# Performance work log

Hardware: AMD Instinct MI355X
Metric: run time of the kernel (lower is better)

The kernel has to match this reference:

```python
import jax, jax.numpy as jnp
import numpy as np

B, S, D, V, OOV = 32, 1024, 512, 50000, 1000
BN_EPS = 1e-5


def setup_inputs() -> dict:
    key = jax.random.key(0)
    ks = jax.random.split(key, 24)
    std = 0.02
    inp = {
        'dec_output': jax.random.normal(ks[0], (B, 1, D), jnp.float32),
        'dec_hid_h': jax.random.normal(ks[1], (1, B, D), jnp.float32),
        'dec_hid_c': jax.random.normal(ks[2], (1, B, D), jnp.float32),
        'dec_inp': jax.random.normal(ks[3], (B, 1, D), jnp.float32),
        'enc_op': jax.random.normal(ks[4], (B, S, 2 * D), jnp.float32),
        'enc_op1': jax.random.normal(ks[5], (B, S, 2 * D), jnp.float32),
        'src_inp': jax.random.randint(ks[6], (B, S), 0, V, jnp.int64) if jax.config.jax_enable_x64 else jax.random.randint(ks[6], (B, S), 0, V, jnp.int32),
        # mod_dec_op: Linear(2D -> 2D) with bias
        'W_dec': jax.random.normal(ks[7], (2 * D, 2 * D), jnp.float32) * std,
        'b_dec': jax.random.normal(ks[8], (2 * D,), jnp.float32) * std,
        # get_attn: Linear(2D -> 1), no bias
        'w_attn': jax.random.normal(ks[9], (2 * D,), jnp.float32) * std,
        # get_vocab: Linear(3D -> D) then Linear(D -> V-OOV)
        'W_v1': jax.random.normal(ks[10], (D, 3 * D), jnp.float32) * std,
        'b_v1': jax.random.normal(ks[11], (D,), jnp.float32) * std,
        'W_v2': jax.random.normal(ks[12], (V - OOV, D), jnp.float32) * std,
        'b_v2': jax.random.normal(ks[13], (V - OOV,), jnp.float32) * std,
        # p_gen: sigmoid(Linear([context(2D); dec_state(2D); dec_inp(D)] -> 1))
        'W_p': jax.random.normal(ks[14], (1, 5 * D), jnp.float32) * std,
        'b_p': jax.random.normal(ks[15], (1,), jnp.float32) * std,
        # BatchNorm1d(2D), eval mode
        'bn_gamma': jnp.ones((2 * D,), jnp.float32),
        'bn_beta': jnp.zeros((2 * D,), jnp.float32),
        'bn_mean': jax.random.normal(ks[16], (2 * D,), jnp.float32) * 0.1,
        'bn_var': jax.random.uniform(ks[17], (2 * D,), jnp.float32, 0.5, 1.5),
    }
    return inp


def reference(dec_output, dec_hid_h, dec_hid_c, dec_inp, enc_op, enc_op1, src_inp,
              W_dec, b_dec, w_attn, W_v1, b_v1, W_v2, b_v2, W_p, b_p,
              bn_gamma, bn_beta, bn_mean, bn_var):
    # dec_op: [B, 2D] = [h_b ; c_b]
    dec_op = jnp.concatenate([dec_hid_h[0], dec_hid_c[0]], axis=-1)
    dec_op1 = dec_op @ W_dec.T + b_dec                              # [B, 2D]
    features = jnp.tanh(enc_op1 + dec_op1[:, None, :])              # [B, S, 2D]
    attn = jax.nn.softmax(jnp.einsum('bsd,d->bs', features, w_attn), axis=-1)
    mask = (src_inp != 0).astype(attn.dtype)
    attn = attn * mask
    attn = attn / jnp.sum(attn, axis=1, keepdims=True)              # renormalize
    context = jnp.einsum('bs,bsd->bd', attn, enc_op)                # [B, 2D]
    context = (context - bn_mean) * jax.lax.rsqrt(bn_var + BN_EPS) * bn_gamma + bn_beta
    temp = jnp.concatenate([dec_output[:, 0, :], context], axis=-1)  # [B, 3D]
    logits = (temp @ W_v1.T + b_v1) @ W_v2.T + b_v2                 # [B, V-OOV]
    p_vocab = jax.nn.softmax(logits, axis=-1)
    p_vocab = jnp.concatenate([p_vocab, jnp.zeros((p_vocab.shape[0], OOV), p_vocab.dtype)], axis=-1)
    pg_in = jnp.concatenate([context, dec_op, dec_inp[:, 0, :]], axis=-1)  # [B, 5D]
    p_gen = jax.nn.sigmoid(pg_in @ W_p.T + b_p)                     # [B, 1]
    src_attn = (1.0 - p_gen) * attn                                  # [B, S]
    p_final = p_gen * p_vocab                                        # [B, V]
    rows = jnp.arange(p_final.shape[0])[:, None]
    p_final = p_final.at[rows, src_inp].add(src_attn)
    p_final = p_final + (p_final == 0).astype(p_final.dtype) * 1e-12
    return (p_final, attn, context)
```

## Files before the change

### kernel.cpp

```cpp
#include <hip/hip_runtime.h>

#define B    32
#define S    1024
#define D    512
#define D2   1024
#define D5   2560
#define V    50000
#define VO   49000
#define NCH  14
#define CHW  3500
#define NCHV 383

__device__ __forceinline__ float fast_tanh(float x){
    float e = __expf(2.0f * x);
    return 1.0f - __fdividef(2.0f, e + 1.0f);
}

__global__ __launch_bounds__(256) void gemm_nt(
    const float* __restrict__ W, int Nreal, int K,
    const float* __restrict__ xa, const float* __restrict__ xb,
    int xsplit, int xstra, int xstrb,
    float* __restrict__ parts, int KS)
{
    __shared__ float sW[16 * 260];
    __shared__ float sX[16 * 32];
    const int t    = threadIdx.x;
    const int lane = t & 63;
    const int v0   = blockIdx.x * 256;
    const int ks0  = blockIdx.y * KS;
    const int b0   = (t >> 6) * 8;

    const int vrow  = v0 + t;
    const size_t wb = (size_t)((vrow < Nreal) ? vrow : (Nreal - 1)) * K;

    float acc[4][8];
    #pragma unroll
    for (int i = 0; i < 4; ++i)
        #pragma unroll
        for (int j = 0; j < 8; ++j) acc[i][j] = 0.f;

    const int  xbi  = t >> 2;
    const int  xq   = t & 3;
    const bool xact = t < 128;

    float4 wreg[4];
    float  xreg[4];
    #pragma unroll
    for (int e = 0; e < 4; ++e) wreg[e] = *(const float4*)&W[wb + ks0 + e * 4];
    if (xact){
        #pragma unroll
        for (int e = 0; e < 4; ++e){
            int k = ks0 + xq * 4 + e;
            xreg[e] = (k < xsplit) ? xa[xbi * xstra + k] : xb[xbi * xstrb + (k - xsplit)];
        }
    }

    const int ntiles = KS >> 4;
    for (int tl = 0; tl < ntiles; ++tl){
        #pragma unroll
        for (int e = 0; e < 4; ++e){
            sW[(e * 4 + 0) * 260 + t] = wreg[e].x;
            sW[(e * 4 + 1) * 260 + t] = wreg[e].y;
            sW[(e * 4 + 2) * 260 + t] = wreg[e].z;
            sW[(e * 4 + 3) * 260 + t] = wreg[e].w;
        }
        if (xact){
            #pragma unroll
            for (int e = 0; e < 4; ++e) sX[(xq * 4 + e) * 32 + xbi] = xreg[e];
        }
        __syncthreads();
        if (tl + 1 < ntiles){
            int kn = ks0 + (tl + 1) * 16;
            #pragma unroll
            for (int e = 0; e < 4; ++e) wreg[e] = *(const float4*)&W[wb + kn + e * 4];
            if (xact){
                #pragma unroll
                for (int e = 0; e < 4; ++e){
                    int k = kn + xq * 4 + e;
                    xreg[e] = (k < xsplit) ? xa[xbi * xstra + k] : xb[xbi * xstrb + (k - xsplit)];
                }
            }
        }
        #pragma unroll
        for (int kk = 0; kk < 16; ++kk){
            const float4 w0 = *(const float4*)&sW[kk * 260 + lane * 4];
            const float4 x0 = *(const float4*)&sX[kk * 32 + b0];
            const float4 x1 = *(const float4*)&sX[kk * 32 + b0 + 4];
            const float wv[4] = {w0.x, w0.y, w0.z, w0.w};
            const float xv[8] = {x0.x, x0.y, x0.z, x0.w, x1.x, x1.y, x1.z, x1.w};
            #pragma unroll
            for (int i = 0; i < 4; ++i)
                #pragma unroll
                for (int j = 0; j < 8; ++j)
                    acc[i][j] += wv[i] * xv[j];
        }
        __syncthreads();
    }
    const int vbase = v0 + lane * 4;
    if (vbase < Nreal){
        const size_t pb = (size_t)blockIdx.y * B;
        #pragma unroll
        for (int j = 0; j < 8; ++j){
            float4 o = make_float4(acc[0][j], acc[1][j], acc[2][j], acc[3][j]);
            *(float4*)&parts[(pb + b0 + j) * (size_t)Nreal + vbase] = o;
        }
    }
}

__global__ void kreduce(const float* __restrict__ parts, float* __restrict__ out,
                        int n, int nsplit, const float* __restrict__ bias, int bmask){
    int i = blockIdx.x * 256 + threadIdx.x;
    if (i < n){
        float s = 0.f;
        for (int p = 0; p < nsplit; ++p) s += parts[(size_t)p * n + i];
        if (bias) s += bias[i & bmask];
        out[i] = s;
    }
}

__global__ __launch_bounds__(256) void gemm_vocab(
    const float* __restrict__ W, const float* __restrict__ hid,
    const float* __restrict__ b2, float* __restrict__ lred,
    float* __restrict__ mch, float* __restrict__ sch)
{
    __shared__ float sW[16 * 132];
    __shared__ float sX[16 * 32];
    const int t    = threadIdx.x;
    const int lane = t & 63;
    const int v0   = blockIdx.x * 128;
    const int b0   = (t >> 6) * 8;

    const int sr   = t & 127;
    const int sh   = (t >> 7) * 8;
    const int vrow = v0 + sr;
    const size_t wb = (size_t)((vrow < VO) ? vrow : (VO - 1)) * D + sh;

    const int  xbi  = t >> 2;
    const int  xq   = (t & 3) * 4;
    const bool xact = t < 128;

    float acc[2][8];
    #pragma unroll
    for (int i = 0; i < 2; ++i)
        #pragma unroll
        for (int j = 0; j < 8; ++j) acc[i][j] = 0.f;

    float4 wreg[2];
    float  xreg[4];
    wreg[0] = *(const float4*)&W[wb];
    wreg[1] = *(const float4*)&W[wb + 4];
    if (xact){
        #pragma unroll
        for (int e = 0; e < 4; ++e) xreg[e] = hid[xbi * D + xq + e];
    }

    for (int tl = 0; tl < 32; ++tl){
        sW[(sh + 0) * 132 + sr] = wreg[0].x;
        sW[(sh + 1) * 132 + sr] = wreg[0].y;
        sW[(sh + 2) * 132 + sr] = wreg[0].z;
        sW[(sh + 3) * 132 + sr] = wreg[0].w;
        sW[(sh + 4) * 132 + sr] = wreg[1].x;
        sW[(sh + 5) * 132 + sr] = wreg[1].y;
        sW[(sh + 6) * 132 + sr] = wreg[1].z;
        sW[(sh + 7) * 132 + sr] = wreg[1].w;
        if (xact){
            #pragma unroll
            for (int e = 0; e < 4; ++e) sX[(xq + e) * 32 + xbi] = xreg[e];
        }
        __syncthreads();
        if (tl + 1 < 32){
            const int kn = (tl + 1) * 16;
            wreg[0] = *(const float4*)&W[wb + kn];
            wreg[1] = *(const float4*)&W[wb + kn + 4];
            if (xact){
                #pragma unroll
                for (int e = 0; e < 4; ++e) xreg[e] = hid[xbi * D + kn + xq + e];
            }
        }
        #pragma unroll
        for (int kk = 0; kk < 16; ++kk){
            const float2 w  = *(const float2*)&sW[kk * 132 + lane * 2];
            const float4 x0 = *(const float4*)&sX[kk * 32 + b0];
            const float4 x1 = *(const float4*)&sX[kk * 32 + b0 + 4];
            const float xv[8] = {x0.x, x0.y, x0.z, x0.w, x1.x, x1.y, x1.z, x1.w};
            #pragma unroll
            for (int j = 0; j < 8; ++j){
                acc[0][j] += w.x * xv[j];
                acc[1][j] += w.y * xv[j];
            }
        }
        __syncthreads();
    }

    const int  va    = v0 + lane * 2;
    const bool valid = va < VO;
    float b2a = 0.f, b2b = 0.f;
    if (valid){ float2 bb = *(const float2*)&b2[va]; b2a = bb.x; b2b = bb.y; }

    #pragma unroll
    for (int j = 0; j < 8; ++j){
        const int b = b0 + j;
        float m, s;
        if (valid){
            float la = acc[0][j] + b2a;
            float lb = acc[1][j] + b2b;
            *(float2*)&lred[(size_t)b * VO + va] = make_float2(la, lb);
            m = fmaxf(la, lb);
            s = __expf(la - m) + __expf(lb - m);
        } else { m = -1e30f; s = 0.f; }
        #pragma unroll
        for (int off = 1; off < 64; off <<= 1){
            float m2 = __shfl_xor(m, off, 64);
            float s2 = __shfl_xor(s, off, 64);
            float M  = fmaxf(m, m2);
            s = s * __expf(m - M) + s2 * __expf(m2 - M);
            m = M;
        }
        if (lane == 0){
            mch[b * NCHV + blockIdx.x] = m;
            sch[b * NCHV + blockIdx.x] = s;
        }
    }
}

__global__ void k2a_logit(const float* __restrict__ enc1, const float* __restrict__ dop1,
                          const float* __restrict__ bdec, const float* __restrict__ wat,
                          float* __restrict__ lg){
    int b = blockIdx.x;
    int wave = threadIdx.x >> 6, lane = threadIdx.x & 63;
    int s0 = blockIdx.y * 16 + wave * 4;
    __shared__ float sd[D2], sw[D2];
    for (int i = threadIdx.x; i < D2; i += 256){
        sd[i] = dop1[b * D2 + i] + bdec[i];
        sw[i] = wat[i];
    }
    __syncthreads();
    const float4* sd4 = (const float4*)sd;
    const float4* sw4 = (const float4*)sw;
    for (int r = 0; r < 4; ++r){
        int s = s0 + r;
        const float4* row = (const float4*)(enc1 + ((size_t)b * S + s) * D2);
        float acc = 0.f;
        #pragma unroll
        for (int i = 0; i < 4; ++i){
            int k4 = i * 64 + lane;
            float4 e = row[k4]; float4 dv = sd4[k4]; float4 wv = sw4[k4];
            acc += fast_tanh(e.x + dv.x) * wv.x + fast_tanh(e.y + dv.y) * wv.y
                 + fast_tanh(e.z + dv.z) * wv.z + fast_tanh(e.w + dv.w) * wv.w;
        }
        #pragma unroll
        for (int off = 32; off > 0; off >>= 1) acc += __shfl_down(acc, off, 64);
        if (lane == 0) lg[b * S + s] = acc;
    }
}

__global__ void k2b_attnsm(const float* __restrict__ lg, const int* __restrict__ src,
                           float* __restrict__ attn){
    int b = blockIdx.x, t = threadIdx.x;
    __shared__ float red[256];
    float l[4];
    float m = -1e30f;
    #pragma unroll
    for (int i = 0; i < 4; ++i){ l[i] = lg[b * S + t + i * 256]; m = fmaxf(m, l[i]); }
    red[t] = m; __syncthreads();
    for (int o = 128; o > 0; o >>= 1){
        if (t < o) red[t] = fmaxf(red[t], red[t + o]);
        __syncthreads();
    }
    m = red[0]; __syncthreads();
    float e[4]; float sum = 0.f;
    #pragma unroll
    for (int i = 0; i < 4; ++i){
        int s = t + i * 256;
        bool keep = src[b * S + s] != 0;
        e[i] = keep ? __expf(l[i] - m) : 0.f;
        sum += e[i];
    }
    red[t] = sum; __syncthreads();
    for (int o = 128; o > 0; o >>= 1){
        if (t < o) red[t] += red[t + o];
        __syncthreads();
    }
    float inv = 1.0f / red[0];
    #pragma unroll
    for (int i = 0; i < 4; ++i) attn[b * S + t + i * 256] = e[i] * inv;
}

__global__ void k2c_ctxpart(const float* __restrict__ enc, const float* __restrict__ attn,
                            float* __restrict__ part){
    int b = blockIdx.x, sp = blockIdx.y, t = threadIdx.x;
    __shared__ float sa[32];
    if (t < 32) sa[t] = attn[b * S + sp * 32 + t];
    __syncthreads();
    const float4* base = (const float4*)(enc + ((size_t)b * S + sp * 32) * D2);
    float4 acc = make_float4(0.f, 0.f, 0.f, 0.f);
    #pragma unroll 4
    for (int s = 0; s < 32; ++s){
        float a = sa[s];
        float4 e = base[s * (D2 / 4) + t];
        acc.x += a * e.x; acc.y += a * e.y; acc.z += a * e.z; acc.w += a * e.w;
    }
    ((float4*)(part + ((size_t)(b * 32 + sp)) * D2))[t] = acc;
}

__global__ void k2d_ctxbn(const float* __restrict__ part, const float* __restrict__ gamma,
                          const float* __restrict__ beta, const float* __restrict__ mean,
                          const float* __restrict__ var, float* __restrict__ ctx){
    int b = blockIdx.x, t = threadIdx.x;
    float4 acc = make_float4(0.f, 0.f, 0.f, 0.f);
    for (int sp = 0; sp < 32; ++sp){
        float4 p = ((const float4*)(part + ((size_t)(b * 32 + sp)) * D2))[t];
        acc.x += p.x; acc.y += p.y; acc.z += p.z; acc.w += p.w;
    }
    float4 g  = ((const float4*)gamma)[t];
    float4 be = ((const float4*)beta)[t];
    float4 mn = ((const float4*)mean)[t];
    float4 vr = ((const float4*)var)[t];
    acc.x = (acc.x - mn.x) * rsqrtf(vr.x + 1e-5f) * g.x + be.x;
    acc.y = (acc.y - mn.y) * rsqrtf(vr.y + 1e-5f) * g.y + be.y;
    acc.z = (acc.z - mn.z) * rsqrtf(vr.z + 1e-5f) * g.z + be.z;
    acc.w = (acc.w - mn.w) * rsqrtf(vr.w + 1e-5f) * g.w + be.w;
    ((float4*)(ctx + (size_t)b * D2))[t] = acc;
}

__global__ void k3b_pgen(const float* __restrict__ ctx, const float* __restrict__ h,
                         const float* __restrict__ c, const float* __restrict__ di,
                         const float* __restrict__ Wp, const float* __restrict__ bp,
                         float* __restrict__ pg){
    int b = blockIdx.x, t = threadIdx.x;
    float acc = 0.f;
    for (int k = t; k < D5; k += 256){
        float x;
        if (k < D2)            x = ctx[b * D2 + k];
        else if (k < D2 + D)   x = h[b * D + (k - D2)];
        else if (k < 2 * D2)   x = c[b * D + (k - D2 - D)];
        else                   x = di[b * D + (k - 2 * D2)];
        acc += x * Wp[k];
    }
    __shared__ float red[256];
    red[t] = acc; __syncthreads();
    for (int o = 128; o > 0; o >>= 1){
        if (t < o) red[t] += red[t + o];
        __syncthreads();
    }
    if (t == 0){
        float z = red[0] + bp[0];
        pg[b] = 1.0f / (1.0f + __expf(-z));
    }
}

__global__ void kB_comb(const float* __restrict__ mch, const float* __restrict__ sch,
                        const float* __restrict__ pg, float* __restrict__ Mb,
                        float* __restrict__ scaleb){
    int b = blockIdx.x, t = threadIdx.x;
    float m = -1e30f, s = 0.f;
    for (int c = t; c < NCHV; c += 128){
        float mc = mch[b * NCHV + c], sc = sch[b * NCHV + c];
        float M = fmaxf(m, mc);
        s = s * __expf(m - M) + sc * __expf(mc - M);
        m = M;
    }
    __shared__ float sm[128], ss[128];
    sm[t] = m; ss[t] = s; __syncthreads();
    for (int o = 64; o > 0; o >>= 1){
        if (t < o){
            float m1 = sm[t], m2 = sm[t + o];
            float M = fmaxf(m1, m2);
            ss[t] = ss[t] * __expf(m1 - M) + ss[t + o] * __expf(m2 - M);
            sm[t] = M;
        }
        __syncthreads();
    }
    if (t == 0){
        Mb[b] = sm[0];
        scaleb[b] = pg[b] / ss[0];
    }
}

__global__ void kC_final(const float* __restrict__ lred, const float* __restrict__ Mb,
                         const float* __restrict__ scaleb, float* __restrict__ pf){
    int b = blockIdx.x, c = blockIdx.y, t = threadIdx.x;
    if (c == NCH){
        for (int v = VO + t; v < V; v += 256) pf[(size_t)b * V + v] = 0.f;
        return;
    }
    float M = Mb[b], sc = scaleb[b];
    for (int v = c * CHW + t; v < (c + 1) * CHW; v += 256)
        pf[(size_t)b * V + v] = sc * __expf(lred[(size_t)b * VO + v] - M);
}

__global__ void k5b_scatter(const int* __restrict__ src, const float* __restrict__ attn,
                            const float* __restrict__ pg, float* __restrict__ pf){
    int b = blockIdx.x, t = threadIdx.x;
    float c1 = 1.0f - pg[b];
    for (int s = t; s < S; s += 256){
        int idx = src[b * S + s];
        atomicAdd(&pf[(size_t)b * V + idx], c1 * attn[b * S + s]);
    }
}

extern "C" void kernel_launch(void* const* d_in, const int* in_sizes, int n_in,
                              void* d_out, int out_size, void* d_ws, size_t ws_size,
                              hipStream_t stream){
    (void)in_sizes; (void)n_in; (void)out_size; (void)ws_size;
    const float* dec_output = (const float*)d_in[0];
    const float* h          = (const float*)d_in[1];
    const float* c          = (const float*)d_in[2];
    const float* dec_inp    = (const float*)d_in[3];
    const float* enc_op     = (const float*)d_in[4];
    const float* enc_op1    = (const float*)d_in[5];
    const int*   src        = (const int*)d_in[6];
    const float* W_dec      = (const float*)d_in[7];
    const float* b_dec      = (const float*)d_in[8];
    const float* w_attn     = (const float*)d_in[9];
    const float* W_v1       = (const float*)d_in[10];
    const float* b_v1       = (const float*)d_in[11];
    const float* W_v2       = (const float*)d_in[12];
    const float* b_v2       = (const float*)d_in[13];
    const float* W_p        = (const float*)d_in[14];
    const float* b_p        = (const float*)d_in[15];
    const float* bn_g       = (const float*)d_in[16];
    const float* bn_b       = (const float*)d_in[17];
    const float* bn_m       = (const float*)d_in[18];
    const float* bn_v       = (const float*)d_in[19];

    float* ws = (float*)d_ws;
    float* p1       = ws;
    float* dec_op1  = ws + 524288;
    float* p3       = ws + 557056;
    float* hidden   = ws + 819200;
    float* lred     = ws + 835584;
    float* attn_lg  = ws + 2403584;
    float* ctx_part = ws + 2436352;
    float* pg       = ws + 3484928;
    float* mch      = ws + 3484960;
    float* sch      = ws + 3497216;
    float* Mb       = ws + 3509472;
    float* scaleb   = ws + 3509504;

    float* pf   = (float*)d_out;
    float* attn = pf + 1600000;
    float* ctx  = pf + 1632768;

    gemm_nt <<<dim3(4, 16),  256, 0, stream>>>(W_dec, D2, D2, h, c, D, D, D, p1, 64);
    kreduce <<<128,          256, 0, stream>>>(p1, dec_op1, B * D2, 16, nullptr, 0);
    k2a_logit<<<dim3(B, 64), 256, 0, stream>>>(enc_op1, dec_op1, b_dec, w_attn, attn_lg);
    k2b_attnsm<<<B,          256, 0, stream>>>(attn_lg, src, attn);
    k2c_ctxpart<<<dim3(B, 32), 256, 0, stream>>>(enc_op, attn, ctx_part);
    k2d_ctxbn<<<B,           256, 0, stream>>>(ctx_part, bn_g, bn_b, bn_m, bn_v, ctx);
    gemm_nt <<<dim3(2, 16),  256, 0, stream>>>(W_v1, D, D + D2, dec_output, ctx,
                                               D, D, D2, p3, 96);
    kreduce <<<64,           256, 0, stream>>>(p3, hidden, B * D, 16, b_v1, D - 1);
    k3b_pgen<<<B,            256, 0, stream>>>(ctx, h, c, dec_inp, W_p, b_p, pg);
    gemm_vocab<<<NCHV,       256, 0, stream>>>(W_v2, hidden, b_v2, lred, mch, sch);
    kB_comb <<<B,            128, 0, stream>>>(mch, sch, pg, Mb, scaleb);
    kC_final<<<dim3(B, NCH + 1), 256, 0, stream>>>(lred, Mb, scaleb, pf);
    k5b_scatter<<<B,         256, 0, stream>>>(src, attn, pg, pf);
}
```

Before: 486.4 us.

## Fuse attention softmax, reduce+pgen and vocab combine; halve vocab GEMM tile

The attention softmax kernel is removed. Per-chunk max and sum partials are now computed inside the logit kernel, and the context kernel combines them itself. The kreduce and p_gen kernels are merged into one launch, and the separate combine kernel is folded into the final softmax-write kernel, which redoes the per-batch reduction in each chunk block. The vocab GEMM now uses 64-row tiles with 128 threads, giving 766 blocks for better CU coverage, at the cost of fewer FMAs per shared load and redundant combine work.

```diff
diff --git a/kernel.cpp b/kernel.cpp
--- a/kernel.cpp
+++ b/kernel.cpp
@@ -9,7 +9,7 @@
 #define VO   49000
 #define NCH  14
 #define CHW  3500
-#define NCHV 383
+#define NCHV 766
 
 __device__ __forceinline__ float fast_tanh(float x){
     float e = __expf(2.0f * x);
@@ -118,118 +118,16 @@
     }
 }
 
-__global__ __launch_bounds__(256) void gemm_vocab(
-    const float* __restrict__ W, const float* __restrict__ hid,
-    const float* __restrict__ b2, float* __restrict__ lred,
-    float* __restrict__ mch, float* __restrict__ sch)
-{
-    __shared__ float sW[16 * 132];
-    __shared__ float sX[16 * 32];
-    const int t    = threadIdx.x;
-    const int lane = t & 63;
-    const int v0   = blockIdx.x * 128;
-    const int b0   = (t >> 6) * 8;
-
-    const int sr   = t & 127;
-    const int sh   = (t >> 7) * 8;
-    const int vrow = v0 + sr;
-    const size_t wb = (size_t)((vrow < VO) ? vrow : (VO - 1)) * D + sh;
-
-    const int  xbi  = t >> 2;
-    const int  xq   = (t & 3) * 4;
-    const bool xact = t < 128;
-
-    float acc[2][8];
-    #pragma unroll
-    for (int i = 0; i < 2; ++i)
-        #pragma unroll
-        for (int j = 0; j < 8; ++j) acc[i][j] = 0.f;
-
-    float4 wreg[2];
-    float  xreg[4];
-    wreg[0] = *(const float4*)&W[wb];
-    wreg[1] = *(const float4*)&W[wb + 4];
-    if (xact){
-        #pragma unroll
-        for (int e = 0; e < 4; ++e) xreg[e] = hid[xbi * D + xq + e];
-    }
-
-    for (int tl = 0; tl < 32; ++tl){
-        sW[(sh + 0) * 132 + sr] = wreg[0].x;
-        sW[(sh + 1) * 132 + sr] = wreg[0].y;
-        sW[(sh + 2) * 132 + sr] = wreg[0].z;
-        sW[(sh + 3) * 132 + sr] = wreg[0].w;
-        sW[(sh + 4) * 132 + sr] = wreg[1].x;
-        sW[(sh + 5) * 132 + sr] = wreg[1].y;
-        sW[(sh + 6) * 132 + sr] = wreg[1].z;
-        sW[(sh + 7) * 132 + sr] = wreg[1].w;
-        if (xact){
-            #pragma unroll
-            for (int e = 0; e < 4; ++e) sX[(xq + e) * 32 + xbi] = xreg[e];
-        }
-        __syncthreads();
-        if (tl + 1 < 32){
-            const int kn = (tl + 1) * 16;
-            wreg[0] = *(const float4*)&W[wb + kn];
-            wreg[1] = *(const float4*)&W[wb + kn + 4];
-            if (xact){
-                #pragma unroll
-                for (int e = 0; e < 4; ++e) xreg[e] = hid[xbi * D + kn + xq + e];
-            }
-        }
-        #pragma unroll
-        for (int kk = 0; kk < 16; ++kk){
-            const float2 w  = *(const float2*)&sW[kk * 132 + lane * 2];
-            const float4 x0 = *(const float4*)&sX[kk * 32 + b0];
-            const float4 x1 = *(const float4*)&sX[kk * 32 + b0 + 4];
-            const float xv[8] = {x0.x, x0.y, x0.z, x0.w, x1.x, x1.y, x1.z, x1.w};
-            #pragma unroll
-            for (int j = 0; j < 8; ++j){
-                acc[0][j] += w.x * xv[j];
-                acc[1][j] += w.y * xv[j];
-            }
-        }
-        __syncthreads();
-    }
-
-    const int  va    = v0 + lane * 2;
-    const bool valid = va < VO;
-    float b2a = 0.f, b2b = 0.f;
-    if (valid){ float2 bb = *(const float2*)&b2[va]; b2a = bb.x; b2b = bb.y; }
-
-    #pragma unroll
-    for (int j = 0; j < 8; ++j){
-        const int b = b0 + j;
-        float m, s;
-        if (valid){
-            float la = acc[0][j] + b2a;
-            float lb = acc[1][j] + b2b;
-            *(float2*)&lred[(size_t)b * VO + va] = make_float2(la, lb);
-            m = fmaxf(la, lb);
-            s = __expf(la - m) + __expf(lb - m);
-        } else { m = -1e30f; s = 0.f; }
-        #pragma unroll
-        for (int off = 1; off < 64; off <<= 1){
-            float m2 = __shfl_xor(m, off, 64);
-            float s2 = __shfl_xor(s, off, 64);
-            float M  = fmaxf(m, m2);
-            s = s * __expf(m - M) + s2 * __expf(m2 - M);
-            m = M;
-        }
-        if (lane == 0){
-            mch[b * NCHV + blockIdx.x] = m;
-            sch[b * NCHV + blockIdx.x] = s;
-        }
-    }
-}
-
 __global__ void k2a_logit(const float* __restrict__ enc1, const float* __restrict__ dop1,
                           const float* __restrict__ bdec, const float* __restrict__ wat,
-                          float* __restrict__ lg){
+                          const int* __restrict__ src,
+                          float* __restrict__ lg, float* __restrict__ pm,
+                          float* __restrict__ ps){
     int b = blockIdx.x;
     int wave = threadIdx.x >> 6, lane = threadIdx.x & 63;
     int s0 = blockIdx.y * 16 + wave * 4;
     __shared__ float sd[D2], sw[D2];
+    __shared__ float slog[16];
     for (int i = threadIdx.x; i < D2; i += 256){
         sd[i] = dop1[b * D2 + i] + bdec[i];
         sw[i] = wat[i];
@@ -250,47 +148,57 @@
         }
         #pragma unroll
         for (int off = 32; off > 0; off >>= 1) acc += __shfl_down(acc, off, 64);
-        if (lane == 0) lg[b * S + s] = acc;
-    }
-}
-
-__global__ void k2b_attnsm(const float* __restrict__ lg, const int* __restrict__ src,
-                           float* __restrict__ attn){
-    int b = blockIdx.x, t = threadIdx.x;
-    __shared__ float red[256];
-    float l[4];
-    float m = -1e30f;
-    #pragma unroll
-    for (int i = 0; i < 4; ++i){ l[i] = lg[b * S + t + i * 256]; m = fmaxf(m, l[i]); }
-    red[t] = m; __syncthreads();
-    for (int o = 128; o > 0; o >>= 1){
-        if (t < o) red[t] = fmaxf(red[t], red[t + o]);
-        __syncthreads();
-    }
-    m = red[0]; __syncthreads();
-    float e[4]; float sum = 0.f;
-    #pragma unroll
-    for (int i = 0; i < 4; ++i){
-        int s = t + i * 256;
-        bool keep = src[b * S + s] != 0;
-        e[i] = keep ? __expf(l[i] - m) : 0.f;
-        sum += e[i];
-    }
-    red[t] = sum; __syncthreads();
-    for (int o = 128; o > 0; o >>= 1){
-        if (t < o) red[t] += red[t + o];
-        __syncthreads();
-    }
-    float inv = 1.0f / red[0];
-    #pragma unroll
-    for (int i = 0; i < 4; ++i) attn[b * S + t + i * 256] = e[i] * inv;
-}
-
-__global__ void k2c_ctxpart(const float* __restrict__ enc, const float* __restrict__ attn,
-                            float* __restrict__ part){
+        if (lane == 0){
+            lg[b * S + s] = acc;
+            slog[wave * 4 + r] = acc;
+        }
+    }
+    __syncthreads();
+    if (threadIdx.x == 0){
+        int sbase = blockIdx.y * 16;
+        float m = -1e30f;
+        #pragma unroll
+        for (int i = 0; i < 16; ++i) m = fmaxf(m, slog[i]);
+        float sum = 0.f;
+        #pragma unroll
+        for (int i = 0; i < 16; ++i){
+            bool keep = src[b * S + sbase + i] != 0;
+            sum += keep ? __expf(slog[i] - m) : 0.f;
+        }
+        pm[b * 64 + blockIdx.y] = m;
+        ps[b * 64 + blockIdx.y] = sum;
+    }
+}
+
+__global__ void k2c_attn_ctx(const float* __restrict__ enc, const float* __restrict__ lg,
+                             const int* __restrict__ src, const float* __restrict__ pm,
+                             const float* __restrict__ ps,
+                             float* __restrict__ attn, float* __restrict__ part){
     int b = blockIdx.x, sp = blockIdx.y, t = threadIdx.x;
     __shared__ float sa[32];
-    if (t < 32) sa[t] = attn[b * S + sp * 32 + t];
+    __shared__ float sMS[2];
+    if (t < 64){
+        float m = pm[b * 64 + t];
+        float s = ps[b * 64 + t];
+        float M = m;
+        #pragma unroll
+        for (int off = 1; off < 64; off <<= 1) M = fmaxf(M, __shfl_xor(M, off, 64));
+        float sv = s * __expf(m - M);
+        #pragma unroll
+        for (int off = 1; off < 64; off <<= 1) sv += __shfl_xor(sv, off, 64);
+        if (t == 0){ sMS[0] = M; sMS[1] = sv; }
+    }
+    __syncthreads();
+    float M   = sMS[0];
+    float inv = 1.0f / sMS[1];
+    if (t < 32){
+        int s = sp * 32 + t;
+        float l = lg[b * S + s];
+        bool keep = src[b * S + s] != 0;
+        float a = keep ? __expf(l - M) * inv : 0.f;
+        attn[b * S + s] = a;
+        sa[t] = a;
+    }
     __syncthreads();
     const float4* base = (const float4*)(enc + ((size_t)b * S + sp * 32) * D2);
     float4 acc = make_float4(0.f, 0.f, 0.f, 0.f);
@@ -323,11 +231,22 @@
     ((float4*)(ctx + (size_t)b * D2))[t] = acc;
 }
 
-__global__ void k3b_pgen(const float* __restrict__ ctx, const float* __restrict__ h,
+__global__ void k3r_pgen(const float* __restrict__ parts, float* __restrict__ out,
+                         const float* __restrict__ bias,
+                         const float* __restrict__ ctx, const float* __restrict__ h,
                          const float* __restrict__ c, const float* __restrict__ di,
                          const float* __restrict__ Wp, const float* __restrict__ bp,
                          float* __restrict__ pg){
-    int b = blockIdx.x, t = threadIdx.x;
+    int t = threadIdx.x;
+    if (blockIdx.x < 64){
+        int i = blockIdx.x * 256 + t;
+        float s = 0.f;
+        for (int p = 0; p < 16; ++p) s += parts[(size_t)p * (B * D) + i];
+        s += bias[i & (D - 1)];
+        out[i] = s;
+        return;
+    }
+    int b = blockIdx.x - 64;
     float acc = 0.f;
     for (int k = t; k < D5; k += 256){
         float x;
@@ -349,20 +268,111 @@
     }
 }
 
-__global__ void kB_comb(const float* __restrict__ mch, const float* __restrict__ sch,
-                        const float* __restrict__ pg, float* __restrict__ Mb,
-                        float* __restrict__ scaleb){
-    int b = blockIdx.x, t = threadIdx.x;
+__global__ __launch_bounds__(128) void gemm_vocab64(
+    const float* __restrict__ W, const float* __restrict__ hid,
+    const float* __restrict__ b2, float* __restrict__ lred,
+    float* __restrict__ mch, float* __restrict__ sch)
+{
+    __shared__ float sW[16 * 68];
+    __shared__ float sX[16 * 32];
+    const int t    = threadIdx.x;
+    const int lane = t & 63;
+    const int wave = t >> 6;
+    const int v0   = blockIdx.x * 64;
+
+    const int sr   = t & 63;
+    const int sh   = (t >> 6) * 8;
+    const int vrow = v0 + sr;
+    const size_t wb = (size_t)((vrow < VO) ? vrow : (VO - 1)) * D + sh;
+
+    const int xbi = t >> 2;
+    const int xq  = (t & 3) * 4;
+
+    float acc[16];
+    #pragma unroll
+    for (int j = 0; j < 16; ++j) acc[j] = 0.f;
+
+    float4 wreg[2];
+    float  xreg[4];
+    wreg[0] = *(const float4*)&W[wb];
+    wreg[1] = *(const float4*)&W[wb + 4];
+    #pragma unroll
+    for (int e = 0; e < 4; ++e) xreg[e] = hid[xbi * D + xq + e];
+
+    for (int tl = 0; tl < 32; ++tl){
+        sW[(sh + 0) * 68 + sr] = wreg[0].x;
+        sW[(sh + 1) * 68 + sr] = wreg[0].y;
+        sW[(sh + 2) * 68 + sr] = wreg[0].z;
+        sW[(sh + 3) * 68 + sr] = wreg[0].w;
+        sW[(sh + 4) * 68 + sr] = wreg[1].x;
+        sW[(sh + 5) * 68 + sr] = wreg[1].y;
+        sW[(sh + 6) * 68 + sr] = wreg[1].z;
+        sW[(sh + 7) * 68 + sr] = wreg[1].w;
+        #pragma unroll
+        for (int e = 0; e < 4; ++e) sX[(xq + e) * 32 + xbi] = xreg[e];
+        __syncthreads();
+        if (tl + 1 < 32){
+            const int kn = (tl + 1) * 16;
+            wreg[0] = *(const float4*)&W[wb + kn];
+            wreg[1] = *(const float4*)&W[wb + kn + 4];
+            #pragma unroll
+            for (int e = 0; e < 4; ++e) xreg[e] = hid[xbi * D + kn + xq + e];
+        }
+        #pragma unroll
+        for (int kk = 0; kk < 16; ++kk){
+            const float  w  = sW[kk * 68 + lane];
+            const float4 x0 = *(const float4*)&sX[kk * 32 + wave * 16 + 0];
+            const float4 x1 = *(const float4*)&sX[kk * 32 + wave * 16 + 4];
+            const float4 x2 = *(const float4*)&sX[kk * 32 + wave * 16 + 8];
+            const float4 x3 = *(const float4*)&sX[kk * 32 + wave * 16 + 12];
+            acc[0]  += w * x0.x; acc[1]  += w * x0.y; acc[2]  += w * x0.z; acc[3]  += w * x0.w;
+            acc[4]  += w * x1.x; acc[5]  += w * x1.y; acc[6]  += w * x1.z; acc[7]  += w * x1.w;
+            acc[8]  += w * x2.x; acc[9]  += w * x2.y; acc[10] += w * x2.z; acc[11] += w * x2.w;
+            acc[12] += w * x3.x; acc[13] += w * x3.y; acc[14] += w * x3.z; acc[15] += w * x3.w;
+        }
+        __syncthreads();
+    }
+
+    const int  va    = v0 + lane;
+    const bool valid = va < VO;
+    const float b2v  = valid ? b2[va] : 0.f;
+
+    #pragma unroll
+    for (int j = 0; j < 16; ++j){
+        const int b = wave * 16 + j;
+        float l = acc[j] + b2v;
+        if (valid) lred[(size_t)b * VO + va] = l;
+        float m = valid ? l : -1e30f;
+        #pragma unroll
+        for (int off = 1; off < 64; off <<= 1) m = fmaxf(m, __shfl_xor(m, off, 64));
+        float sv = valid ? __expf(l - m) : 0.f;
+        #pragma unroll
+        for (int off = 1; off < 64; off <<= 1) sv += __shfl_xor(sv, off, 64);
+        if (lane == 0){
+            mch[b * NCHV + blockIdx.x] = m;
+            sch[b * NCHV + blockIdx.x] = sv;
+        }
+    }
+}
+
+__global__ void kC_final2(const float* __restrict__ lred, const float* __restrict__ mch,
+                          const float* __restrict__ sch, const float* __restrict__ pg,
+                          float* __restrict__ pf){
+    int b = blockIdx.x, c = blockIdx.y, t = threadIdx.x;
+    if (c == NCH){
+        for (int v = VO + t; v < V; v += 256) pf[(size_t)b * V + v] = 0.f;
+        return;
+    }
+    __shared__ float sm[256], ss[256];
     float m = -1e30f, s = 0.f;
-    for (int c = t; c < NCHV; c += 128){
-        float mc = mch[b * NCHV + c], sc = sch[b * NCHV + c];
+    for (int ch = t; ch < NCHV; ch += 256){
+        float mc = mch[b * NCHV + ch], sc = sch[b * NCHV + ch];
         float M = fmaxf(m, mc);
         s = s * __expf(m - M) + sc * __expf(mc - M);
         m = M;
     }
-    __shared__ float sm[128], ss[128];
     sm[t] = m; ss[t] = s; __syncthreads();
-    for (int o = 64; o > 0; o >>= 1){
+    for (int o = 128; o > 0; o >>= 1){
         if (t < o){
             float m1 = sm[t], m2 = sm[t + o];
             float M = fmaxf(m1, m2);
@@ -371,20 +381,8 @@
         }
         __syncthreads();
     }
-    if (t == 0){
-        Mb[b] = sm[0];
-        scaleb[b] = pg[b] / ss[0];
-    }
-}
-
-__global__ void kC_final(const float* __restrict__ lred, const float* __restrict__ Mb,
-                         const float* __restrict__ scaleb, float* __restrict__ pf){
-    int b = blockIdx.x, c = blockIdx.y, t = threadIdx.x;
-    if (c == NCH){
-        for (int v = VO + t; v < V; v += 256) pf[(size_t)b * V + v] = 0.f;
-        return;
-    }
-    float M = Mb[b], sc = scaleb[b];
+    float M  = sm[0];
+    float sc = pg[b] / ss[0];
     for (int v = c * CHW + t; v < (c + 1) * CHW; v += 256)
         pf[(size_t)b * V + v] = sc * __expf(lred[(size_t)b * VO + v] - M);
 }
@@ -434,9 +432,9 @@
     float* ctx_part = ws + 2436352;
     float* pg       = ws + 3484928;
     float* mch      = ws + 3484960;
-    float* sch      = ws + 3497216;
-    float* Mb       = ws + 3509472;
-    float* scaleb   = ws + 3509504;
+    float* sch      = ws + 3509472;
+    float* pm       = ws + 3533984;
+    float* ps       = ws + 3536032;
 
     float* pf   = (float*)d_out;
     float* attn = pf + 1600000;
@@ -444,16 +442,16 @@
 
     gemm_nt <<<dim3(4, 16),  256, 0, stream>>>(W_dec, D2, D2, h, c, D, D, D, p1, 64);
     kreduce <<<128,          256, 0, stream>>>(p1, dec_op1, B * D2, 16, nullptr, 0);
-    k2a_logit<<<dim3(B, 64), 256, 0, stream>>>(enc_op1, dec_op1, b_dec, w_attn, attn_lg);
-    k2b_attnsm<<<B,          256, 0, stream>>>(attn_lg, src, attn);
-    k2c_ctxpart<<<dim3(B, 32), 256, 0, stream>>>(enc_op, attn, ctx_part);
+    k2a_logit<<<dim3(B, 64), 256, 0, stream>>>(enc_op1, dec_op1, b_dec, w_attn, src,
+                                               attn_lg, pm, ps);
+    k2c_attn_ctx<<<dim3(B, 32), 256, 0, stream>>>(enc_op, attn_lg, src, pm, ps,
+                                                  attn, ctx_part);
     k2d_ctxbn<<<B,           256, 0, stream>>>(ctx_part, bn_g, bn_b, bn_m, bn_v, ctx);
     gemm_nt <<<dim3(2, 16),  256, 0, stream>>>(W_v1, D, D + D2, dec_output, ctx,
                                                D, D, D2, p3, 96);
-    kreduce <<<64,           256, 0, stream>>>(p3, hidden, B * D, 16, b_v1, D - 1);
-    k3b_pgen<<<B,            256, 0, stream>>>(ctx, h, c, dec_inp, W_p, b_p, pg);
-    gemm_vocab<<<NCHV,       256, 0, stream>>>(W_v2, hidden, b_v2, lred, mch, sch);
-    kB_comb <<<B,            128, 0, stream>>>(mch, sch, pg, Mb, scaleb);
-    kC_final<<<dim3(B, NCH + 1), 256, 0, stream>>>(lred, Mb, scaleb, pf);
+    k3r_pgen<<<96,           256, 0, stream>>>(p3, hidden, b_v1,
+                                               ctx, h, c, dec_inp, W_p, b_p, pg);
+    gemm_vocab64<<<NCHV,     128, 0, stream>>>(W_v2, hidden, b_v2, lred, mch, sch);
+    kC_final2<<<dim3(B, NCH + 1), 256, 0, stream>>>(lred, mch, sch, pg, pf);
     k5b_scatter<<<B,         256, 0, stream>>>(src, attn, pg, pf);
 }
```

Result: slower. 506.8 us (+4.2%).
